# Kernel optimization log

Hardware: AMD Instinct MI355X
Metric: run time of the kernel (lower is better)

Reference implementation:

```python
import jax, jax.numpy as jnp
import numpy as np

STATE_LEN = 128
SEQ_LEN = 2048
NUM_ITERS = 2
DIM_IN = 1024
DIM_H = 64
BATCH = 2
T_TOTAL = SEQ_LEN + 2 * STATE_LEN  # 2304
NEG = -1e30  # large-negative causal mask (avoids -inf NaNs under autodiff)


def _ln(x, g, b):
    m = jnp.mean(x, axis=-1, keepdims=True)
    v = jnp.var(x, axis=-1, keepdims=True)
    return (x - m) / jnp.sqrt(v + 1e-5) * g + b


def setup_inputs() -> dict:
    key = jax.random.key(0)
    ks = jax.random.split(key, 16)

    def w(k, fi, fo):
        # torch nn.Linear-style fan-in scaled init (keeps logits O(1))
        return jax.random.normal(k, (fi, fo), jnp.float32) / np.sqrt(fi)

    return {
        "x": jax.random.normal(ks[0], (BATCH, T_TOTAL, DIM_IN), jnp.float32),
        "Wh": w(ks[1], DIM_IN, DIM_H),
        "Whs": w(ks[2], DIM_IN, DIM_H),
        "Whe": w(ks[3], DIM_IN, DIM_H),
        "Wk": w(ks[4], DIM_H, DIM_H),
        "Wq": w(ks[5], DIM_H, DIM_H),
        "Wv": w(ks[6], DIM_H, DIM_H),
        "Wks": w(ks[7], DIM_H, DIM_H),
        "Wqs": w(ks[8], DIM_H, DIM_H),
        "Wvs": w(ks[9], DIM_H, DIM_H),
        "Wke": w(ks[10], DIM_H, DIM_H),
        "Wqe": w(ks[11], DIM_H, DIM_H),
        "Wve": w(ks[12], DIM_H, DIM_H),
        "ln_g": jnp.ones((DIM_IN,), jnp.float32),
        "ln_b": jnp.zeros((DIM_IN,), jnp.float32),
        "ln_gs": jnp.ones((DIM_IN,), jnp.float32),
        "ln_bs": jnp.zeros((DIM_IN,), jnp.float32),
        "ln_ge": jnp.ones((DIM_IN,), jnp.float32),
        "ln_be": jnp.zeros((DIM_IN,), jnp.float32),
        "cope_emb": jax.random.normal(ks[13], (DIM_H, T_TOTAL), jnp.float32),
    }


def reference(x, Wh, Whs, Whe, Wk, Wq, Wv, Wks, Wqs, Wvs, Wke, Wqe, Wve,
              ln_g, ln_b, ln_gs, ln_bs, ln_ge, ln_be, cope_emb):
    S = STATE_LEN
    # extract_state: [state_start | seq | state_end] along token dim
    xs, xm, xe = x[:, :S], x[:, S:-S], x[:, -S:]
    xm = _ln(xm, ln_g, ln_b)
    xs = _ln(xs, ln_gs, ln_bs)
    xe = _ln(xe, ln_ge, ln_be)

    mem = xm @ Wh                 # (B, L, D)
    mem_s = xs @ Whs              # (B, S, D)
    mem_e = xe @ Whe              # (B, S, D)

    scale = 1.0 / np.sqrt(DIM_H)  # xformers default scale (beta=None)
    tril = jnp.tril(jnp.ones((T_TOTAL, T_TOTAL), bool))
    mask = jnp.where(tril, 0.0, NEG)  # log of lower-triangular ones

    mem_full = None
    for ix in range(NUM_ITERS):
        k = jnp.concatenate([mem_s @ Wks, mem @ Wk, mem_e @ Wke], axis=1)  # (B,T,D)
        q = jnp.concatenate([mem_s @ Wqs, mem @ Wq, mem_e @ Wqe], axis=1)
        v = jnp.concatenate([mem_s @ Wvs, mem @ Wv, mem_e @ Wve], axis=1)

        logits = jnp.einsum('btd,bsd->bts', q, k)  # unscaled, as in CoPE gates
        if ix == 0:
            # CoPE: sigmoid-gated reverse cumsum positions + interpolated embedding bias
            gates = jax.nn.sigmoid(logits)
            pos = jnp.flip(jnp.cumsum(jnp.flip(gates, -1), axis=-1), -1)
            pos = jnp.minimum(pos, float(T_TOTAL - 1))
            pos_floor = jnp.floor(pos)
            pos_ceil = jnp.ceil(pos)
            logits_int = jnp.einsum('btd,dn->btn', q, cope_emb)  # (B,T,T)
            lc = jnp.take_along_axis(logits_int, pos_ceil.astype(jnp.int32), axis=-1)
            lf = jnp.take_along_axis(logits_int, pos_floor.astype(jnp.int32), axis=-1)
            wfrac = pos - pos_floor
            bias = lc * wfrac + lf * (1.0 - wfrac)
            scores = logits * scale + mask + bias
        else:
            scores = logits * scale + mask

        attn = jax.nn.softmax(scores, axis=-1)
        mem_full = jnp.einsum('bts,bsd->btd', attn, v)  # (B,T,D)
        if ix < NUM_ITERS - 1:
            mem_s, mem, mem_e = mem_full[:, :S], mem_full[:, S:-S], mem_full[:, -S:]
    return mem_full
```

## Files before the change

kernel.cpp:

```cpp
#include <hip/hip_runtime.h>

#define T_TOT 2304
#define S_LEN 128
#define D_IN  1024
#define D_H   64
#define BATCH 2
#define NROW  (BATCH * T_TOT)
#define CH    (T_TOT / 256)
#define SCALE 0.125f
#define KCHUNKS 8
#define KCW   (D_IN / KCHUNKS)

typedef unsigned short u16;
typedef __attribute__((ext_vector_type(8))) short short8;
typedef __attribute__((ext_vector_type(4))) float f32x4;
typedef __attribute__((ext_vector_type(4))) unsigned short u16x4;

static __device__ __forceinline__ u16 f2bf(float f) {
    unsigned u = __float_as_uint(f);
    unsigned r = (u + 0x7fffu + ((u >> 16) & 1u)) >> 16;
    return (u16)r;
}
static __device__ __forceinline__ float bf2f(u16 s) {
    return __uint_as_float((unsigned)s << 16);
}

__global__ __launch_bounds__(256) void k_ln(
    const float* __restrict__ x,
    const float* __restrict__ ln_g,  const float* __restrict__ ln_b,
    const float* __restrict__ ln_gs, const float* __restrict__ ln_bs,
    const float* __restrict__ ln_ge, const float* __restrict__ ln_be,
    u16* __restrict__ xn_hi, u16* __restrict__ xn_lo)
{
    __shared__ float red1[256], red2[256];
    const int row = blockIdx.x;
    const int t = row % T_TOT;
    const int tid = threadIdx.x;

    const float *gg, *bb;
    if (t < S_LEN)               { gg = ln_gs; bb = ln_bs; }
    else if (t >= T_TOT - S_LEN) { gg = ln_ge; bb = ln_be; }
    else                         { gg = ln_g;  bb = ln_b;  }

    const float4 xv = *(const float4*)(x + (size_t)row * D_IN + 4 * tid);
    float s  = xv.x + xv.y + xv.z + xv.w;
    float s2 = xv.x * xv.x + xv.y * xv.y + xv.z * xv.z + xv.w * xv.w;
    red1[tid] = s; red2[tid] = s2; __syncthreads();
    for (int off = 128; off > 0; off >>= 1) {
        if (tid < off) { red1[tid] += red1[tid + off]; red2[tid] += red2[tid + off]; }
        __syncthreads();
    }
    const float mean = red1[0] * (1.f / D_IN);
    const float var  = red2[0] * (1.f / D_IN) - mean * mean;
    const float rstd = rsqrtf(var + 1e-5f);

    const float4 gv = *(const float4*)(gg + 4 * tid);
    const float4 bv = *(const float4*)(bb + 4 * tid);
    float o0 = (xv.x - mean) * rstd * gv.x + bv.x;
    float o1 = (xv.y - mean) * rstd * gv.y + bv.y;
    float o2 = (xv.z - mean) * rstd * gv.z + bv.z;
    float o3 = (xv.w - mean) * rstd * gv.w + bv.w;

    u16x4 hv, lv;
    hv[0] = f2bf(o0); lv[0] = f2bf(o0 - bf2f(hv[0]));
    hv[1] = f2bf(o1); lv[1] = f2bf(o1 - bf2f(hv[1]));
    hv[2] = f2bf(o2); lv[2] = f2bf(o2 - bf2f(hv[2]));
    hv[3] = f2bf(o3); lv[3] = f2bf(o3 - bf2f(hv[3]));
    *(u16x4*)(xn_hi + (size_t)row * D_IN + 4 * tid) = hv;
    *(u16x4*)(xn_lo + (size_t)row * D_IN + 4 * tid) = lv;
}

__global__ __launch_bounds__(256) void k_wprep(
    const float* __restrict__ Wh, const float* __restrict__ Whs, const float* __restrict__ Whe,
    u16* __restrict__ wT_hi, u16* __restrict__ wT_lo)
{
    const int gid = blockIdx.x * 256 + threadIdx.x;
    const int seg = gid >> 16;
    const int o = gid & 65535;
    const int j = o >> 10, k = o & 1023;
    const float* W = seg == 0 ? Wh : (seg == 1 ? Whs : Whe);
    const float f = W[k * D_H + j];
    const u16 hi = f2bf(f);
    wT_hi[gid] = hi;
    wT_lo[gid] = f2bf(f - bf2f(hi));
}

__global__ __launch_bounds__(256) void k_hgemm(
    const u16* __restrict__ xn_hi, const u16* __restrict__ xn_lo,
    const u16* __restrict__ wT_hi, const u16* __restrict__ wT_lo,
    float* __restrict__ h_part)
{
    const int tile = blockIdx.x;
    const int kc   = blockIdx.y;
    const int k0   = kc * KCW;
    const int tt = tile % 36;
    const int seg = tt < 2 ? 1 : (tt >= 34 ? 2 : 0);

    __shared__ u16 Bh[64 * KCW];
    __shared__ u16 Bl[64 * KCW];

    const int tid = threadIdx.x;
    {
        const int r = tid >> 2;
        const int c0 = (tid & 3) * 32;
        const u16* sh = wT_hi + ((size_t)seg * D_H + r) * D_IN + k0 + c0;
        const u16* sl = wT_lo + ((size_t)seg * D_H + r) * D_IN + k0 + c0;
        const int sw = (r & 7) << 3;
        #pragma unroll
        for (int u = 0; u < 4; ++u) {
            const int col = c0 + 8 * u;
            *(short8*)&Bh[r * KCW + (col ^ sw)] = *(const short8*)(sh + 8 * u);
            *(short8*)&Bl[r * KCW + (col ^ sw)] = *(const short8*)(sl + 8 * u);
        }
    }
    __syncthreads();

    const int w = tid >> 6;
    const int lane = tid & 63;
    const int l15 = lane & 15, lg4 = lane >> 4;
    const int row0 = tile * 64 + w * 16;

    const size_t abase = (size_t)(row0 + l15) * D_IN + k0 + 8 * lg4;
    f32x4 acc[4] = {};

    #pragma unroll
    for (int kk = 0; kk < KCW / 32; ++kk) {
        short8 ah = *(const short8*)(xn_hi + abase + kk * 32);
        short8 al = *(const short8*)(xn_lo + abase + kk * 32);
        #pragma unroll
        for (int j = 0; j < 4; ++j) {
            const int brow = j * 16 + l15;
            const int col = (kk * 32 + 8 * lg4) ^ ((brow & 7) << 3);
            short8 bh = *(const short8*)&Bh[brow * KCW + col];
            short8 bl = *(const short8*)&Bl[brow * KCW + col];
            acc[j] = __builtin_amdgcn_mfma_f32_16x16x32_bf16(al, bh, acc[j], 0, 0, 0);
            acc[j] = __builtin_amdgcn_mfma_f32_16x16x32_bf16(ah, bl, acc[j], 0, 0, 0);
            acc[j] = __builtin_amdgcn_mfma_f32_16x16x32_bf16(ah, bh, acc[j], 0, 0, 0);
        }
    }
    float* hp = h_part + (size_t)kc * ((size_t)NROW * D_H);
    #pragma unroll
    for (int j = 0; j < 4; ++j)
        #pragma unroll
        for (int r = 0; r < 4; ++r)
            hp[(size_t)(row0 + 4 * lg4 + r) * D_H + j * 16 + l15] = acc[j][r];
}

__global__ __launch_bounds__(256) void k_hred(
    const float* __restrict__ h_part, float* __restrict__ h)
{
    const size_t idx = (size_t)blockIdx.x * 256 + threadIdx.x;
    const size_t N = (size_t)NROW * D_H;
    float s = 0.f;
    #pragma unroll
    for (int kc = 0; kc < KCHUNKS; ++kc) s += h_part[kc * N + idx];
    h[idx] = s;
}

template <bool SPLIT>
__global__ __launch_bounds__(192) void k_qkv(
    const float* __restrict__ hin,
    const float* __restrict__ Wk,  const float* __restrict__ Wq,  const float* __restrict__ Wv,
    const float* __restrict__ Wks, const float* __restrict__ Wqs, const float* __restrict__ Wvs,
    const float* __restrict__ Wke, const float* __restrict__ Wqe, const float* __restrict__ Wve,
    u16* __restrict__ q_hi, u16* __restrict__ q_lo,
    u16* __restrict__ k_hi, u16* __restrict__ k_lo,
    u16* __restrict__ vT)
{
    __shared__ float hr[D_H];
    const int bid = blockIdx.x;
    const int b = bid / T_TOT, t = bid % T_TOT;
    const int tid = threadIdx.x;

    const float* hrow = hin + ((size_t)b * T_TOT + t) * D_H;
    if (tid < D_H) hr[tid] = hrow[tid];
    __syncthreads();

    const int which = tid >> 6, j = tid & 63;
    const float* W;
    if (t < S_LEN)               W = which == 0 ? Wks : (which == 1 ? Wqs : Wvs);
    else if (t >= T_TOT - S_LEN) W = which == 0 ? Wke : (which == 1 ? Wqe : Wve);
    else                         W = which == 0 ? Wk  : (which == 1 ? Wq  : Wv);

    float acc = 0.f;
    #pragma unroll
    for (int d = 0; d < D_H; ++d) acc += hr[d] * W[d * D_H + j];

    const size_t idx = ((size_t)b * T_TOT + t) * D_H + j;
    u16 hi = f2bf(acc);
    if (which == 0) {
        k_hi[idx] = hi;
        if (SPLIT) k_lo[idx] = f2bf(acc - bf2f(hi));
    } else if (which == 1) {
        q_hi[idx] = hi;
        if (SPLIT) q_lo[idx] = f2bf(acc - bf2f(hi));
    } else {
        vT[((size_t)b * D_H + j) * T_TOT + t] = hi;
    }
}

__global__ __launch_bounds__(256) void k_copeT(
    const float* __restrict__ cope, u16* __restrict__ cT_hi, u16* __restrict__ cT_lo)
{
    int idx = blockIdx.x * 256 + threadIdx.x;
    int n = idx >> 6, d = idx & 63;
    float f = cope[(size_t)d * T_TOT + n];
    u16 hi = f2bf(f);
    cT_hi[idx] = hi;
    cT_lo[idx] = f2bf(f - bf2f(hi));
}

template <int TERMS, bool CAUSAL>
__global__ __launch_bounds__(256) void k_score(
    const u16* __restrict__ a_hi, const u16* __restrict__ a_lo,
    const u16* __restrict__ b_hi, const u16* __restrict__ b_lo,
    long b_batch_stride,
    float* __restrict__ out)
{
    const int b  = blockIdx.z;
    const int s0 = blockIdx.x * 128;
    if (CAUSAL && s0 > blockIdx.y * 64 + 63) return;
    const int t0 = blockIdx.y * 64 + (threadIdx.x >> 6) * 16;
    const int lane = threadIdx.x & 63;
    const int l15 = lane & 15, lg4 = lane >> 4;

    const size_t a_off = ((size_t)(b * T_TOT + t0 + l15)) * D_H + 8 * lg4;
    short8 ah0 = *(const short8*)(a_hi + a_off);
    short8 ah1 = *(const short8*)(a_hi + a_off + 32);
    short8 al0 = {}, al1 = {};
    if (TERMS == 3) {
        al0 = *(const short8*)(a_lo + a_off);
        al1 = *(const short8*)(a_lo + a_off + 32);
    }

    const u16* bh = b_hi + (size_t)b * b_batch_stride;
    const u16* bl = b_lo + (size_t)b * b_batch_stride;

    float* orow = out + ((size_t)(b * T_TOT + t0 + 4 * lg4)) * T_TOT + s0 + l15;

    #pragma unroll
    for (int ni = 0; ni < 8; ++ni) {
        const size_t b_off = ((size_t)(s0 + ni * 16 + l15)) * D_H + 8 * lg4;
        short8 bh0 = *(const short8*)(bh + b_off);
        short8 bh1 = *(const short8*)(bh + b_off + 32);
        f32x4 acc = {0.f, 0.f, 0.f, 0.f};
        if (TERMS == 3) {
            short8 bl0 = *(const short8*)(bl + b_off);
            short8 bl1 = *(const short8*)(bl + b_off + 32);
            acc = __builtin_amdgcn_mfma_f32_16x16x32_bf16(al0, bh0, acc, 0, 0, 0);
            acc = __builtin_amdgcn_mfma_f32_16x16x32_bf16(al1, bh1, acc, 0, 0, 0);
            acc = __builtin_amdgcn_mfma_f32_16x16x32_bf16(ah0, bl0, acc, 0, 0, 0);
            acc = __builtin_amdgcn_mfma_f32_16x16x32_bf16(ah1, bl1, acc, 0, 0, 0);
        }
        acc = __builtin_amdgcn_mfma_f32_16x16x32_bf16(ah0, bh0, acc, 0, 0, 0);
        acc = __builtin_amdgcn_mfma_f32_16x16x32_bf16(ah1, bh1, acc, 0, 0, 0);
        #pragma unroll
        for (int r = 0; r < 4; ++r)
            orow[(size_t)r * T_TOT + ni * 16] = acc[r];
    }
}

__global__ __launch_bounds__(256) void k_pv(
    const float* __restrict__ pbuf, const u16* __restrict__ vT,
    float* __restrict__ out)
{
    const int b  = blockIdx.z;
    const int t0 = blockIdx.x * 16;
    const int j0 = (threadIdx.x >> 6) * 16;
    const int lane = threadIdx.x & 63;
    const int l15 = lane & 15, lg4 = lane >> 4;

    const u16* pb = (const u16*)pbuf;
    const size_t prow = ((size_t)(b * T_TOT + t0 + l15)) * (2 * (size_t)T_TOT);
    const u16* vrow = vT + ((size_t)(b * D_H + j0 + l15)) * T_TOT;

    f32x4 acc = {0.f, 0.f, 0.f, 0.f};
    const int kmax = t0 + 15;
    for (int sc = 0; sc <= kmax; sc += 32) {
        const int off = sc + 8 * lg4;
        short8 a  = *(const short8*)(pb + prow + off);
        short8 bf = *(const short8*)(vrow + off);
        acc = __builtin_amdgcn_mfma_f32_16x16x32_bf16(a, bf, acc, 0, 0, 0);
    }
    float* obase = out + ((size_t)(b * T_TOT + t0 + 4 * lg4)) * D_H + j0 + l15;
    #pragma unroll
    for (int r = 0; r < 4; ++r) obase[(size_t)r * D_H] = acc[r];
}

template <bool COPE>
__global__ __launch_bounds__(256) void k_erow(
    const float* __restrict__ logits,
    const float* __restrict__ lint,
    float* __restrict__ pbase)
{
    __shared__ float lg[T_TOT];
    __shared__ float red[256];
    __shared__ float extra[COPE ? 2 * T_TOT : 2];

    const int row = blockIdx.x;
    const int t = row % T_TOT;
    const int tid = threadIdx.x;
    const float* lrow = logits + (size_t)row * T_TOT;

    if (COPE) {
        for (int r = 0; r < CH; ++r) { int s = tid + 256 * r; lg[s] = lrow[s]; }
    } else {
        for (int r = 0; r < CH; ++r) { int s = tid + 256 * r; if (s <= t) lg[s] = lrow[s]; }
    }
    __syncthreads();

    if (COPE) {
        const int base = tid * CH;
        float gv[CH];
        float lsum = 0.f;
        #pragma unroll
        for (int u = 0; u < CH; ++u) {
            float g = 1.f / (1.f + expf(-lg[base + u]));
            gv[u] = g;
            lsum += g;
        }
        red[tid] = lsum; __syncthreads();
        for (int off = 1; off < 256; off <<= 1) {
            float tv = (tid >= off) ? red[tid - off] : 0.f;
            __syncthreads();
            red[tid] += tv;
            __syncthreads();
        }
        const float total = red[255];
        float run = red[tid] - lsum;
        #pragma unroll
        for (int u = 0; u < CH; ++u) {
            float p = fminf(total - run, (float)(T_TOT - 1));
            extra[base + u] = p;
            run += gv[u];
        }
        const float* lintrow = lint + (size_t)row * T_TOT;
        for (int r = 0; r < CH; ++r) { int s = tid + 256 * r; extra[T_TOT + s] = lintrow[s]; }
        __syncthreads();
    }

    float scv[CH];
    float mx = -3.4e38f;
    for (int r = 0; r < CH; ++r) {
        int sidx = tid + 256 * r;
        float sc = -3.4e38f;
        if (sidx <= t) {
            sc = lg[sidx] * SCALE;
            if (COPE) {
                float p = extra[sidx];
                float pf = floorf(p);
                int fi = (int)pf;
                int ci = (int)ceilf(p);
                float w = p - pf;
                sc += extra[T_TOT + ci] * w + extra[T_TOT + fi] * (1.f - w);
            }
            mx = fmaxf(mx, sc);
        }
        scv[r] = sc;
    }
    __syncthreads();
    red[tid] = mx; __syncthreads();
    for (int off = 128; off > 0; off >>= 1) {
        if (tid < off) red[tid] = fmaxf(red[tid], red[tid + off]);
        __syncthreads();
    }
    mx = red[0];
    __syncthreads();

    float pvv[CH];
    float psum = 0.f;
    for (int r = 0; r < CH; ++r) {
        int sidx = tid + 256 * r;
        float pv = 0.f;
        if (sidx <= t) { pv = expf(scv[r] - mx); psum += pv; }
        pvv[r] = pv;
    }
    red[tid] = psum; __syncthreads();
    for (int off = 128; off > 0; off >>= 1) {
        if (tid < off) red[tid] += red[tid + off];
        __syncthreads();
    }
    const float inv = 1.f / red[0];

    u16* prow = (u16*)(pbase + (size_t)row * T_TOT);
    for (int r = 0; r < CH; ++r) {
        int sidx = tid + 256 * r;
        prow[sidx] = f2bf(pvv[r] * inv);
    }
}

extern "C" void kernel_launch(void* const* d_in, const int* in_sizes, int n_in,
                              void* d_out, int out_size, void* d_ws, size_t ws_size,
                              hipStream_t stream) {
    const float* x    = (const float*)d_in[0];
    const float* Wh   = (const float*)d_in[1];
    const float* Whs  = (const float*)d_in[2];
    const float* Whe  = (const float*)d_in[3];
    const float* Wk   = (const float*)d_in[4];
    const float* Wq   = (const float*)d_in[5];
    const float* Wv   = (const float*)d_in[6];
    const float* Wks  = (const float*)d_in[7];
    const float* Wqs  = (const float*)d_in[8];
    const float* Wvs  = (const float*)d_in[9];
    const float* Wke  = (const float*)d_in[10];
    const float* Wqe  = (const float*)d_in[11];
    const float* Wve  = (const float*)d_in[12];
    const float* ln_g  = (const float*)d_in[13];
    const float* ln_b  = (const float*)d_in[14];
    const float* ln_gs = (const float*)d_in[15];
    const float* ln_bs = (const float*)d_in[16];
    const float* ln_ge = (const float*)d_in[17];
    const float* ln_be = (const float*)d_in[18];
    const float* cope  = (const float*)d_in[19];

    float* out = (float*)d_out;

    const size_t N = (size_t)NROW * D_H;
    char* W = (char*)d_ws;
    u16* xn_hi  = (u16*)W;    W += (size_t)NROW * D_IN * 2;
    u16* xn_lo  = (u16*)W;    W += (size_t)NROW * D_IN * 2;
    u16* wT_hi  = (u16*)W;    W += (size_t)3 * D_H * D_IN * 2;
    u16* wT_lo  = (u16*)W;    W += (size_t)3 * D_H * D_IN * 2;
    float* h    = (float*)W;  W += N * 4;
    u16* q_hi   = (u16*)W;    W += N * 2;
    u16* q_lo   = (u16*)W;    W += N * 2;
    u16* k_hi   = (u16*)W;    W += N * 2;
    u16* k_lo   = (u16*)W;    W += N * 2;
    u16* vT     = (u16*)W;    W += N * 2;
    u16* cT_hi  = (u16*)W;    W += (size_t)T_TOT * D_H * 2;
    u16* cT_lo  = (u16*)W;    W += (size_t)T_TOT * D_H * 2;
    float* logits = (float*)W; W += (size_t)BATCH * T_TOT * T_TOT * 4;
    float* lint   = (float*)W; W += (size_t)BATCH * T_TOT * T_TOT * 4;
    float* mem1   = (float*)W;

    float* h_part = lint;

    const dim3 sg(T_TOT / 128, T_TOT / 64, BATCH);
    const long kstride = (long)T_TOT * D_H;

    k_ln<<<NROW, 256, 0, stream>>>(x, ln_g, ln_b, ln_gs, ln_bs, ln_ge, ln_be,
                                   xn_hi, xn_lo);
    k_wprep<<<768, 256, 0, stream>>>(Wh, Whs, Whe, wT_hi, wT_lo);
    k_copeT<<<(T_TOT * D_H) / 256, 256, 0, stream>>>(cope, cT_hi, cT_lo);
    k_hgemm<<<dim3(NROW / 64, KCHUNKS), 256, 0, stream>>>(xn_hi, xn_lo, wT_hi, wT_lo, h_part);
    k_hred<<<(int)(N / 256), 256, 0, stream>>>(h_part, h);

    k_qkv<true><<<NROW, 192, 0, stream>>>(h, Wk, Wq, Wv, Wks, Wqs, Wvs, Wke, Wqe, Wve,
                                          q_hi, q_lo, k_hi, k_lo, vT);
    k_score<3, false><<<sg, 256, 0, stream>>>(q_hi, q_lo, k_hi, k_lo, kstride, logits);
    k_score<3, false><<<sg, 256, 0, stream>>>(q_hi, q_lo, cT_hi, cT_lo, 0, lint);
    k_erow<true><<<NROW, 256, 0, stream>>>(logits, lint, lint);
    k_pv<<<dim3(T_TOT / 16, 1, BATCH), 256, 0, stream>>>(lint, vT, mem1);

    k_qkv<false><<<NROW, 192, 0, stream>>>(mem1, Wk, Wq, Wv, Wks, Wqs, Wvs, Wke, Wqe, Wve,
                                           q_hi, q_lo, k_hi, k_lo, vT);
    k_score<1, true><<<sg, 256, 0, stream>>>(q_hi, q_lo, k_hi, k_lo, kstride, logits);
    k_erow<false><<<NROW, 256, 0, stream>>>(logits, nullptr, lint);
    k_pv<<<dim3(T_TOT / 16, 1, BATCH), 256, 0, stream>>>(lint, vT, out);
}
```

Baseline: 209.8 us.

## Fuse prep and score launches, unroll PV loop, use wave-shuffle reductions in softmax

Merges the weight and CoPE-embedding transpose kernels into one launch, and merges the two first-iteration score GEMMs (q·k and q·cope) into one kernel that reuses the loaded q fragments. The PV kernel now issues four independent MFMA accumulator chains per step to hide load and MFMA latency. The softmax/CoPE row kernel replaces shared-memory tree scans and reductions with wavefront shuffles plus a 4-entry cross-wave combine, removing many barriers. Launch overhead and synchronization drop, at the cost of a larger fused score kernel with more registers.

```diff
diff --git a/kernel.cpp b/kernel.cpp
--- a/kernel.cpp
+++ b/kernel.cpp
@@ -70,19 +70,33 @@
     *(u16x4*)(xn_lo + (size_t)row * D_IN + 4 * tid) = lv;
 }
 
-__global__ __launch_bounds__(256) void k_wprep(
+#define WPREP_N (3 * D_H * D_IN)
+__global__ __launch_bounds__(256) void k_prep(
     const float* __restrict__ Wh, const float* __restrict__ Whs, const float* __restrict__ Whe,
-    u16* __restrict__ wT_hi, u16* __restrict__ wT_lo)
+    const float* __restrict__ cope,
+    u16* __restrict__ wT_hi, u16* __restrict__ wT_lo,
+    u16* __restrict__ cT_hi, u16* __restrict__ cT_lo)
 {
     const int gid = blockIdx.x * 256 + threadIdx.x;
-    const int seg = gid >> 16;
-    const int o = gid & 65535;
-    const int j = o >> 10, k = o & 1023;
-    const float* W = seg == 0 ? Wh : (seg == 1 ? Whs : Whe);
-    const float f = W[k * D_H + j];
-    const u16 hi = f2bf(f);
-    wT_hi[gid] = hi;
-    wT_lo[gid] = f2bf(f - bf2f(hi));
+    if (gid < WPREP_N) {
+        const int seg = gid >> 16;
+        const int o = gid & 65535;
+        const int j = o >> 10, k = o & 1023;
+        const float* W = seg == 0 ? Wh : (seg == 1 ? Whs : Whe);
+        const float f = W[k * D_H + j];
+        const u16 hi = f2bf(f);
+        wT_hi[gid] = hi;
+        wT_lo[gid] = f2bf(f - bf2f(hi));
+    } else {
+        const int idx = gid - WPREP_N;
+        if (idx < T_TOT * D_H) {
+            const int n = idx >> 6, d = idx & 63;
+            const float f = cope[(size_t)d * T_TOT + n];
+            const u16 hi = f2bf(f);
+            cT_hi[idx] = hi;
+            cT_lo[idx] = f2bf(f - bf2f(hi));
+        }
+    }
 }
 
 __global__ __launch_bounds__(256) void k_hgemm(
@@ -199,43 +213,70 @@
     }
 }
 
-__global__ __launch_bounds__(256) void k_copeT(
-    const float* __restrict__ cope, u16* __restrict__ cT_hi, u16* __restrict__ cT_lo)
-{
-    int idx = blockIdx.x * 256 + threadIdx.x;
-    int n = idx >> 6, d = idx & 63;
-    float f = cope[(size_t)d * T_TOT + n];
-    u16 hi = f2bf(f);
-    cT_hi[idx] = hi;
-    cT_lo[idx] = f2bf(f - bf2f(hi));
-}
-
-template <int TERMS, bool CAUSAL>
-__global__ __launch_bounds__(256) void k_score(
+__global__ __launch_bounds__(256) void k_score2(
     const u16* __restrict__ a_hi, const u16* __restrict__ a_lo,
-    const u16* __restrict__ b_hi, const u16* __restrict__ b_lo,
-    long b_batch_stride,
-    float* __restrict__ out)
+    const u16* __restrict__ k_hi, const u16* __restrict__ k_lo,
+    const u16* __restrict__ c_hi, const u16* __restrict__ c_lo,
+    float* __restrict__ logits, float* __restrict__ lint)
 {
     const int b  = blockIdx.z;
     const int s0 = blockIdx.x * 128;
-    if (CAUSAL && s0 > blockIdx.y * 64 + 63) return;
     const int t0 = blockIdx.y * 64 + (threadIdx.x >> 6) * 16;
     const int lane = threadIdx.x & 63;
     const int l15 = lane & 15, lg4 = lane >> 4;
 
     const size_t a_off = ((size_t)(b * T_TOT + t0 + l15)) * D_H + 8 * lg4;
+    const short8 ah0 = *(const short8*)(a_hi + a_off);
+    const short8 ah1 = *(const short8*)(a_hi + a_off + 32);
+    const short8 al0 = *(const short8*)(a_lo + a_off);
+    const short8 al1 = *(const short8*)(a_lo + a_off + 32);
+
+    const size_t orow_off = ((size_t)(b * T_TOT + t0 + 4 * lg4)) * T_TOT + s0 + l15;
+
+    const u16* bh = k_hi + (size_t)b * (T_TOT * D_H);
+    const u16* bl = k_lo + (size_t)b * (T_TOT * D_H);
+    float* o = logits + orow_off;
+    #pragma unroll
+    for (int pass = 0; pass < 2; ++pass) {
+        #pragma unroll
+        for (int ni = 0; ni < 8; ++ni) {
+            const size_t b_off = ((size_t)(s0 + ni * 16 + l15)) * D_H + 8 * lg4;
+            short8 bh0 = *(const short8*)(bh + b_off);
+            short8 bh1 = *(const short8*)(bh + b_off + 32);
+            short8 bl0 = *(const short8*)(bl + b_off);
+            short8 bl1 = *(const short8*)(bl + b_off + 32);
+            f32x4 acc = {0.f, 0.f, 0.f, 0.f};
+            acc = __builtin_amdgcn_mfma_f32_16x16x32_bf16(al0, bh0, acc, 0, 0, 0);
+            acc = __builtin_amdgcn_mfma_f32_16x16x32_bf16(al1, bh1, acc, 0, 0, 0);
+            acc = __builtin_amdgcn_mfma_f32_16x16x32_bf16(ah0, bl0, acc, 0, 0, 0);
+            acc = __builtin_amdgcn_mfma_f32_16x16x32_bf16(ah1, bl1, acc, 0, 0, 0);
+            acc = __builtin_amdgcn_mfma_f32_16x16x32_bf16(ah0, bh0, acc, 0, 0, 0);
+            acc = __builtin_amdgcn_mfma_f32_16x16x32_bf16(ah1, bh1, acc, 0, 0, 0);
+            #pragma unroll
+            for (int r = 0; r < 4; ++r)
+                o[(size_t)r * T_TOT + ni * 16] = acc[r];
+        }
+        bh = c_hi; bl = c_lo;
+        o = lint + orow_off;
+    }
+}
+
+__global__ __launch_bounds__(256) void k_score(
+    const u16* __restrict__ a_hi, const u16* __restrict__ b_hi,
+    float* __restrict__ out)
+{
+    const int b  = blockIdx.z;
+    const int s0 = blockIdx.x * 128;
+    if (s0 > blockIdx.y * 64 + 63) return;
+    const int t0 = blockIdx.y * 64 + (threadIdx.x >> 6) * 16;
+    const int lane = threadIdx.x & 63;
+    const int l15 = lane & 15, lg4 = lane >> 4;
+
+    const size_t a_off = ((size_t)(b * T_TOT + t0 + l15)) * D_H + 8 * lg4;
     short8 ah0 = *(const short8*)(a_hi + a_off);
     short8 ah1 = *(const short8*)(a_hi + a_off + 32);
-    short8 al0 = {}, al1 = {};
-    if (TERMS == 3) {
-        al0 = *(const short8*)(a_lo + a_off);
-        al1 = *(const short8*)(a_lo + a_off + 32);
-    }
-
-    const u16* bh = b_hi + (size_t)b * b_batch_stride;
-    const u16* bl = b_lo + (size_t)b * b_batch_stride;
-
+
+    const u16* bh = b_hi + (size_t)b * (T_TOT * D_H);
     float* orow = out + ((size_t)(b * T_TOT + t0 + 4 * lg4)) * T_TOT + s0 + l15;
 
     #pragma unroll
@@ -244,14 +285,6 @@
         short8 bh0 = *(const short8*)(bh + b_off);
         short8 bh1 = *(const short8*)(bh + b_off + 32);
         f32x4 acc = {0.f, 0.f, 0.f, 0.f};
-        if (TERMS == 3) {
-            short8 bl0 = *(const short8*)(bl + b_off);
-            short8 bl1 = *(const short8*)(bl + b_off + 32);
-            acc = __builtin_amdgcn_mfma_f32_16x16x32_bf16(al0, bh0, acc, 0, 0, 0);
-            acc = __builtin_amdgcn_mfma_f32_16x16x32_bf16(al1, bh1, acc, 0, 0, 0);
-            acc = __builtin_amdgcn_mfma_f32_16x16x32_bf16(ah0, bl0, acc, 0, 0, 0);
-            acc = __builtin_amdgcn_mfma_f32_16x16x32_bf16(ah1, bl1, acc, 0, 0, 0);
-        }
         acc = __builtin_amdgcn_mfma_f32_16x16x32_bf16(ah0, bh0, acc, 0, 0, 0);
         acc = __builtin_amdgcn_mfma_f32_16x16x32_bf16(ah1, bh1, acc, 0, 0, 0);
         #pragma unroll
@@ -270,18 +303,33 @@
     const int lane = threadIdx.x & 63;
     const int l15 = lane & 15, lg4 = lane >> 4;
 
-    const u16* pb = (const u16*)pbuf;
-    const size_t prow = ((size_t)(b * T_TOT + t0 + l15)) * (2 * (size_t)T_TOT);
-    const u16* vrow = vT + ((size_t)(b * D_H + j0 + l15)) * T_TOT;
-
-    f32x4 acc = {0.f, 0.f, 0.f, 0.f};
-    const int kmax = t0 + 15;
-    for (int sc = 0; sc <= kmax; sc += 32) {
-        const int off = sc + 8 * lg4;
-        short8 a  = *(const short8*)(pb + prow + off);
-        short8 bf = *(const short8*)(vrow + off);
-        acc = __builtin_amdgcn_mfma_f32_16x16x32_bf16(a, bf, acc, 0, 0, 0);
-    }
+    const u16* pb = (const u16*)pbuf
+        + ((size_t)(b * T_TOT + t0 + l15)) * (2 * (size_t)T_TOT) + 8 * lg4;
+    const u16* vb = vT + ((size_t)(b * D_H + j0 + l15)) * T_TOT + 8 * lg4;
+
+    f32x4 a0 = {}, a1 = {}, a2 = {}, a3 = {};
+    const int smax = t0 + 16;
+    int sc = 0;
+    for (; sc + 128 <= smax; sc += 128) {
+        short8 p0 = *(const short8*)(pb + sc);
+        short8 v0 = *(const short8*)(vb + sc);
+        short8 p1 = *(const short8*)(pb + sc + 32);
+        short8 v1 = *(const short8*)(vb + sc + 32);
+        short8 p2 = *(const short8*)(pb + sc + 64);
+        short8 v2 = *(const short8*)(vb + sc + 64);
+        short8 p3 = *(const short8*)(pb + sc + 96);
+        short8 v3 = *(const short8*)(vb + sc + 96);
+        a0 = __builtin_amdgcn_mfma_f32_16x16x32_bf16(p0, v0, a0, 0, 0, 0);
+        a1 = __builtin_amdgcn_mfma_f32_16x16x32_bf16(p1, v1, a1, 0, 0, 0);
+        a2 = __builtin_amdgcn_mfma_f32_16x16x32_bf16(p2, v2, a2, 0, 0, 0);
+        a3 = __builtin_amdgcn_mfma_f32_16x16x32_bf16(p3, v3, a3, 0, 0, 0);
+    }
+    for (; sc < smax; sc += 32) {
+        short8 p0 = *(const short8*)(pb + sc);
+        short8 v0 = *(const short8*)(vb + sc);
+        a0 = __builtin_amdgcn_mfma_f32_16x16x32_bf16(p0, v0, a0, 0, 0, 0);
+    }
+    f32x4 acc = (a0 + a1) + (a2 + a3);
     float* obase = out + ((size_t)(b * T_TOT + t0 + 4 * lg4)) * D_H + j0 + l15;
     #pragma unroll
     for (int r = 0; r < 4; ++r) obase[(size_t)r * D_H] = acc[r];
@@ -294,12 +342,13 @@
     float* __restrict__ pbase)
 {
     __shared__ float lg[T_TOT];
-    __shared__ float red[256];
     __shared__ float extra[COPE ? 2 * T_TOT : 2];
+    __shared__ float wtot[4], wmax[4], wsum[4];
 
     const int row = blockIdx.x;
     const int t = row % T_TOT;
     const int tid = threadIdx.x;
+    const int lane = tid & 63, wid = tid >> 6;
     const float* lrow = logits + (size_t)row * T_TOT;
 
     if (COPE) {
@@ -319,18 +368,25 @@
             gv[u] = g;
             lsum += g;
         }
-        red[tid] = lsum; __syncthreads();
-        for (int off = 1; off < 256; off <<= 1) {
-            float tv = (tid >= off) ? red[tid - off] : 0.f;
-            __syncthreads();
-            red[tid] += tv;
-            __syncthreads();
-        }
-        const float total = red[255];
-        float run = red[tid] - lsum;
+        float cs = lsum;
+        #pragma unroll
+        for (int off = 1; off < 64; off <<= 1) {
+            float n = __shfl_up(cs, off);
+            if (lane >= off) cs += n;
+        }
+        if (lane == 63) wtot[wid] = cs;
+        __syncthreads();
+        float pre = 0.f, tot = 0.f;
+        #pragma unroll
+        for (int w = 0; w < 4; ++w) {
+            float vv = wtot[w];
+            tot += vv;
+            if (w < wid) pre += vv;
+        }
+        float run = pre + cs - lsum;
         #pragma unroll
         for (int u = 0; u < CH; ++u) {
-            float p = fminf(total - run, (float)(T_TOT - 1));
+            float p = fminf(tot - run, (float)(T_TOT - 1));
             extra[base + u] = p;
             run += gv[u];
         }
@@ -341,6 +397,7 @@
 
     float scv[CH];
     float mx = -3.4e38f;
+    #pragma unroll
     for (int r = 0; r < CH; ++r) {
         int sidx = tid + 256 * r;
         float sc = -3.4e38f;
@@ -358,31 +415,29 @@
         }
         scv[r] = sc;
     }
+    #pragma unroll
+    for (int off = 32; off > 0; off >>= 1) mx = fmaxf(mx, __shfl_xor(mx, off));
+    if (lane == 0) wmax[wid] = mx;
     __syncthreads();
-    red[tid] = mx; __syncthreads();
-    for (int off = 128; off > 0; off >>= 1) {
-        if (tid < off) red[tid] = fmaxf(red[tid], red[tid + off]);
-        __syncthreads();
-    }
-    mx = red[0];
-    __syncthreads();
+    mx = fmaxf(fmaxf(wmax[0], wmax[1]), fmaxf(wmax[2], wmax[3]));
 
     float pvv[CH];
     float psum = 0.f;
+    #pragma unroll
     for (int r = 0; r < CH; ++r) {
         int sidx = tid + 256 * r;
         float pv = 0.f;
         if (sidx <= t) { pv = expf(scv[r] - mx); psum += pv; }
         pvv[r] = pv;
     }
-    red[tid] = psum; __syncthreads();
-    for (int off = 128; off > 0; off >>= 1) {
-        if (tid < off) red[tid] += red[tid + off];
-        __syncthreads();
-    }
-    const float inv = 1.f / red[0];
+    #pragma unroll
+    for (int off = 32; off > 0; off >>= 1) psum += __shfl_xor(psum, off);
+    if (lane == 0) wsum[wid] = psum;
+    __syncthreads();
+    const float inv = 1.f / (wsum[0] + wsum[1] + wsum[2] + wsum[3]);
 
     u16* prow = (u16*)(pbase + (size_t)row * T_TOT);
+    #pragma unroll
     for (int r = 0; r < CH; ++r) {
         int sidx = tid + 256 * r;
         prow[sidx] = f2bf(pvv[r] * inv);
@@ -436,25 +491,23 @@
     float* h_part = lint;
 
     const dim3 sg(T_TOT / 128, T_TOT / 64, BATCH);
-    const long kstride = (long)T_TOT * D_H;
 
     k_ln<<<NROW, 256, 0, stream>>>(x, ln_g, ln_b, ln_gs, ln_bs, ln_ge, ln_be,
                                    xn_hi, xn_lo);
-    k_wprep<<<768, 256, 0, stream>>>(Wh, Whs, Whe, wT_hi, wT_lo);
-    k_copeT<<<(T_TOT * D_H) / 256, 256, 0, stream>>>(cope, cT_hi, cT_lo);
+    k_prep<<<(WPREP_N + T_TOT * D_H + 255) / 256, 256, 0, stream>>>(
+        Wh, Whs, Whe, cope, wT_hi, wT_lo, cT_hi, cT_lo);
     k_hgemm<<<dim3(NROW / 64, KCHUNKS), 256, 0, stream>>>(xn_hi, xn_lo, wT_hi, wT_lo, h_part);
     k_hred<<<(int)(N / 256), 256, 0, stream>>>(h_part, h);
 
     k_qkv<true><<<NROW, 192, 0, stream>>>(h, Wk, Wq, Wv, Wks, Wqs, Wvs, Wke, Wqe, Wve,
                                           q_hi, q_lo, k_hi, k_lo, vT);
-    k_score<3, false><<<sg, 256, 0, stream>>>(q_hi, q_lo, k_hi, k_lo, kstride, logits);
-    k_score<3, false><<<sg, 256, 0, stream>>>(q_hi, q_lo, cT_hi, cT_lo, 0, lint);
+    k_score2<<<sg, 256, 0, stream>>>(q_hi, q_lo, k_hi, k_lo, cT_hi, cT_lo, logits, lint);
     k_erow<true><<<NROW, 256, 0, stream>>>(logits, lint, lint);
     k_pv<<<dim3(T_TOT / 16, 1, BATCH), 256, 0, stream>>>(lint, vT, mem1);
 
     k_qkv<false><<<NROW, 192, 0, stream>>>(mem1, Wk, Wq, Wv, Wks, Wqs, Wvs, Wke, Wqe, Wve,
                                            q_hi, q_lo, k_hi, k_lo, vT);
-    k_score<1, true><<<sg, 256, 0, stream>>>(q_hi, q_lo, k_hi, k_lo, kstride, logits);
+    k_score<<<sg, 256, 0, stream>>>(q_hi, k_hi, logits);
     k_erow<false><<<NROW, 256, 0, stream>>>(logits, nullptr, lint);
     k_pv<<<dim3(T_TOT / 16, 1, BATCH), 256, 0, stream>>>(lint, vT, out);
 }
```

Result: faster. 189.4 us (-9.7%).
